# Performance work log

Measured on AMD Instinct MI355X. Metric: run time of the kernel, lower is better.

The kernel has to match this reference:

```python
import jax, jax.numpy as jnp
import numpy as np
import math

EPS = 1e-6
BN_EPS = 1e-5
PI2 = 2.0 * math.pi
NBASIS = 10


def setup_inputs() -> dict:
    key = jax.random.key(0)
    ks = jax.random.split(key, 12)
    nb, nc, ng, ch, npar, out_ch = 4, 512, 2048, 3, 3, 64
    return {
        "x_c": jax.random.normal(ks[0], (nb, nc, ch), jnp.float32),
        "y_c": jax.random.normal(ks[1], (nb, nc, ch), jnp.float32),
        "x_g": jax.random.normal(ks[2], (nb, ng, ch), jnp.float32),
        "sigma": jnp.log(1e-4 + 0.1 * jax.random.uniform(ks[3], (npar,), jnp.float32)),
        "mu": jnp.zeros((npar,), jnp.float32),
        "eps1": jax.random.normal(ks[4], (nb, NBASIS, npar), jnp.float32),
        "b_u": jax.random.uniform(ks[5], (nb, NBASIS, npar), jnp.float32),
        "random_w": jax.random.normal(ks[6], (NBASIS,), jnp.float32),
        "conv_w1": 0.1 * jax.random.normal(ks[7], (ch, 1, 3), jnp.float32),
        "conv_b1": jnp.zeros((ch,), jnp.float32),
        "conv_w2": 0.1 * jax.random.normal(ks[8], (ch, 1, 5), jnp.float32),
        "conv_b2": jnp.zeros((ch,), jnp.float32),
        "conv_w3": 0.1 * jax.random.normal(ks[9], (ch, 1, 9), jnp.float32),
        "conv_b3": jnp.zeros((ch,), jnp.float32),
        "bn_gamma": jnp.ones((npar, ch), jnp.float32),
        "bn_beta": jnp.zeros((npar, ch), jnp.float32),
        "g_w": (1.0 / np.sqrt(2 * npar * ch)) * jax.random.normal(ks[10], (out_ch, 2 * npar * ch), jnp.float32),
        "g_b": jnp.zeros((out_ch,), jnp.float32),
    }


def _dwconv1d(x, w, b, pad):
    # x: (nb, ch, L), w: (ch, 1, ksz) depthwise (groups=ch), cross-correlation like torch
    ch = x.shape[1]
    y = jax.lax.conv_general_dilated(
        x, w, window_strides=(1,), padding=[(pad, pad)],
        dimension_numbers=("NCH", "OIH", "NCH"), feature_group_count=ch)
    return y + b[None, :, None]


def _batchnorm1d(x, gamma, beta):
    # training-mode BN over (batch, length) per channel; x: (nb, ch, L)
    m = x.mean(axis=(0, 2), keepdims=True)
    v = x.var(axis=(0, 2), keepdims=True)  # biased variance (torch normalization)
    return gamma[None, :, None] * (x - m) * jax.lax.rsqrt(v + BN_EPS) + beta[None, :, None]


def reference(x_c, y_c, x_g, sigma, mu, eps1, b_u, random_w,
              conv_w1, conv_b1, conv_w2, conv_b2, conv_w3, conv_b3,
              bn_gamma, bn_beta, g_w, g_b):
    nb, nc, ch = x_c.shape
    ng = x_g.shape[1]
    npar = sigma.shape[0]
    scales = jnp.exp(sigma)  # (npar,)

    # RBF pairwise weights: (nb, nc, ng, ch, npar)
    d = (x_c[:, :, None, :, None] - x_g[:, None, :, :, None]) / (scales + EPS)
    wt = jnp.exp(-0.5 * d * d)
    h0 = wt.sum(axis=1)                                   # (nb, ng, ch, npar)
    h1 = jnp.einsum("bngcp,bnc->bgcp", wt, y_c)           # (nb, ng, ch, npar)
    n_h1 = h1 / (h0 + EPS)

    # random Fourier prior on the grid
    w_mu = jnp.exp(mu)
    w_std = 1.0 / (jnp.exp(sigma) + EPS)
    sample_w = w_mu[None, None, :] + w_std[None, None, :] * eps1  # (nb, nbasis, npar)
    sample_b = PI2 * b_u                                          # (nb, nbasis, npar)
    # Psi: (nb, ng, nbasis, ch, npar)
    psi = jnp.cos(sample_w[:, None, :, None, :] * x_g[:, :, None, :, None]
                  + sample_b[:, None, :, None, :])
    fourier_prior = np.sqrt(2.0 / NBASIS) * jnp.einsum("bgkcp,k->bgcp", psi, random_w)

    n_h1_pos = n_h1 + fourier_prior                        # (nb, ng, ch, npar)

    conv_ws = (conv_w1, conv_w2, conv_w3)
    conv_bs = (conv_b1, conv_b2, conv_b3)
    pads = (1, 2, 4)
    cols = []
    for j in range(npar):
        x = jnp.transpose(n_h1_pos[:, :, :, j], (0, 2, 1))  # (nb, ch, ng)
        x = _dwconv1d(x, conv_ws[j], conv_bs[j], pads[j])
        x = _batchnorm1d(x, bn_gamma[j], bn_beta[j])
        cols.append(jnp.transpose(x, (0, 2, 1)))            # (nb, ng, ch)
    n_h1_pos = jnp.stack(cols, axis=-1)                     # (nb, ng, ch, npar)

    h0_f = h0.reshape(nb, ng, -1)
    n_f = n_h1_pos.reshape(nb, ng, -1)
    feat = jnp.concatenate([h0_f, n_f], axis=-1)            # (nb, ng, 2*ch*npar)
    y_out = feat @ g_w.T + g_b                              # (nb, ng, out_channels)
    return (y_out, n_f, fourier_prior, n_h1, h0_f)
```

## Files before the change

kernel.cpp:

```cpp
#include <hip/hip_runtime.h>
#include <math.h>

#define EPS 1e-6f
#define BN_EPSF 1e-5f
#define PI2F 6.2831853071795864769f
#define LOG2EF 1.4426950408889634f
#define NBB 4
#define NCC 512
#define NGG 2048
#define OUTC 64
#define NBAS 10

#define Y_OFF   0
#define NF_OFF  (NBB*NGG*OUTC)
#define FP_OFF  (NF_OFF  + NBB*NGG*9)
#define NH1_OFF (FP_OFF  + NBB*NGG*9)
#define H0_OFF  (NH1_OFF + NBB*NGG*9)

#define WS_PRE   0
#define WS_CONV  (NBB*9*NGG)
#define WS_STATS (2*NBB*9*NGG)

#if defined(__has_builtin)
# if __has_builtin(__builtin_amdgcn_exp2f)
#  define EXP2F(x) __builtin_amdgcn_exp2f(x)
# endif
#endif
#ifndef EXP2F
# define EXP2F(x) exp2f(x)
#endif

__global__ __launch_bounds__(256) void k1_rbf(
    const float* __restrict__ x_c, const float* __restrict__ y_c,
    const float* __restrict__ x_g, const float* __restrict__ sigma,
    const float* __restrict__ mu, const float* __restrict__ eps1,
    const float* __restrict__ b_u, const float* __restrict__ random_w,
    float* __restrict__ out, float* __restrict__ ws)
{
    const int bid = blockIdx.x;
    const int b = bid >> 8;
    const int gtile = bid & 255;
    const int g0 = gtile * 8;
    const int tid = threadIdx.x;

    __shared__ float cxy[NCC*8 + (NCC/32)*4];
    __shared__ float red[32][8][19];
    __shared__ float sw_l[NBAS*3], sb_l[NBAS*3], rw_l[NBAS];

    const float* xcb = x_c + b*NCC*3;
    const float* ycb = y_c + b*NCC*3;
    for (int i = tid; i < NCC*3; i += 256) {
        int n = i/3, c = i - n*3;
        int base = n*8 + ((n>>5)<<2);
        cxy[base + 2*c]     = xcb[i];
        cxy[base + 2*c + 1] = ycb[i];
    }
    if (tid < NBAS*3) {
        int k = tid/3, p = tid - k*3;
        float wmu  = expf(mu[p]);
        float wstd = 1.0f / (expf(sigma[p]) + EPS);
        sw_l[tid] = wmu + wstd * eps1[(b*NBAS + k)*3 + p];
        sb_l[tid] = PI2F * b_u[(b*NBAS + k)*3 + p];
    }
    if (tid < NBAS) rw_l[tid] = random_w[tid];

    float coef[3];
    #pragma unroll
    for (int p = 0; p < 3; ++p) {
        float s = expf(sigma[p]) + EPS;
        coef[p] = (-0.5f * LOG2EF) / (s*s);
    }

    const int gA = tid & 7;
    const int cA = tid >> 3;
    const float xg0 = x_g[(b*NGG + g0 + gA)*3 + 0];
    const float xg1 = x_g[(b*NGG + g0 + gA)*3 + 1];
    const float xg2 = x_g[(b*NGG + g0 + gA)*3 + 2];

    __syncthreads();

    float h0a[3][3] = {{0}}, h1a[3][3] = {{0}};
    const int fbase = cA*128 + ((cA>>1)<<2);
    #pragma unroll 4
    for (int i = 0; i < 16; ++i) {
        float4 A = *(const float4*)&cxy[fbase + i*8];
        float4 B = *(const float4*)&cxy[fbase + i*8 + 4];
        float d0 = A.x - xg0, d1 = A.z - xg1, d2 = B.x - xg2;
        float dx2[3] = {d0*d0, d1*d1, d2*d2};
        float yv[3]  = {A.y, A.w, B.y};
        #pragma unroll
        for (int c = 0; c < 3; ++c)
            #pragma unroll
            for (int p = 0; p < 3; ++p) {
                float w = EXP2F(dx2[c] * coef[p]);
                h0a[c][p] += w;
                h1a[c][p] += w * yv[c];
            }
    }
    #pragma unroll
    for (int c = 0; c < 3; ++c)
        #pragma unroll
        for (int p = 0; p < 3; ++p) {
            red[cA][gA][c*3 + p]     = h0a[c][p];
            red[cA][gA][9 + c*3 + p] = h1a[c][p];
        }
    __syncthreads();

    if (tid < 72) {
        int gl = tid / 9, cp = tid - gl*9;
        int c = cp / 3, p = cp - c*3;
        float h0 = 0.f, h1 = 0.f;
        #pragma unroll 8
        for (int q = 0; q < 32; ++q) {
            h0 += red[q][gl][cp];
            h1 += red[q][gl][9 + cp];
        }
        float nh1 = h1 / (h0 + EPS);
        float xg = x_g[(b*NGG + g0 + gl)*3 + c];
        float fp = 0.f;
        #pragma unroll
        for (int k = 0; k < NBAS; ++k) {
            float arg = __fadd_rn(__fmul_rn(sw_l[k*3 + p], xg), sb_l[k*3 + p]);
            fp += rw_l[k] * cosf(arg);
        }
        fp *= 0.44721359549995793f;
        int base = (b*NGG + g0 + gl)*9 + cp;
        out[H0_OFF  + base] = h0;
        out[NH1_OFF + base] = nh1;
        out[FP_OFF  + base] = fp;
        ws[WS_PRE + (b*9 + cp)*NGG + g0 + gl] = nh1 + fp;
    }
}

__global__ __launch_bounds__(256) void k2_conv(
    const float* __restrict__ cw1, const float* __restrict__ cb1,
    const float* __restrict__ cw2, const float* __restrict__ cb2,
    const float* __restrict__ cw3, const float* __restrict__ cb3,
    float* __restrict__ ws)
{
    int bid = blockIdx.x;
    int b = bid / 72; int r = bid - b*72;
    int cp = r / 8;  int gc = r - cp*8;
    int g = gc*256 + threadIdx.x;
    int c = cp / 3, p = cp - c*3;
    const float* pre = ws + WS_PRE + (b*9 + cp)*NGG;

    int K, pad; const float* w; float bias;
    if (p == 0)      { K = 3; pad = 1; w = cw1 + c*3; bias = cb1[c]; }
    else if (p == 1) { K = 5; pad = 2; w = cw2 + c*5; bias = cb2[c]; }
    else             { K = 9; pad = 4; w = cw3 + c*9; bias = cb3[c]; }

    float acc = bias;
    for (int k = 0; k < K; ++k) {
        int idx = g - pad + k;
        if (idx >= 0 && idx < NGG) acc += w[k] * pre[idx];
    }
    ws[WS_CONV + (b*9 + cp)*NGG + g] = acc;

    float s1 = acc, s2 = acc*acc;
    #pragma unroll
    for (int o = 32; o > 0; o >>= 1) {
        s1 += __shfl_down(s1, o);
        s2 += __shfl_down(s2, o);
    }
    __shared__ float r1[4], r2[4];
    int lane = threadIdx.x & 63, wv = threadIdx.x >> 6;
    if (lane == 0) { r1[wv] = s1; r2[wv] = s2; }
    __syncthreads();
    if (threadIdx.x == 0) {
        float t1 = r1[0] + r1[1] + r1[2] + r1[3];
        float t2 = r2[0] + r2[1] + r2[2] + r2[3];
        int pidx = cp*32 + b*8 + gc;
        ws[WS_STATS + pidx*2]     = t1;
        ws[WS_STATS + pidx*2 + 1] = t2;
    }
}

__global__ __launch_bounds__(256) void k3_out(
    const float* __restrict__ bn_gamma, const float* __restrict__ bn_beta,
    const float* __restrict__ g_w, const float* __restrict__ g_b,
    float* __restrict__ out, float* __restrict__ ws)
{
    __shared__ float gw_l[OUTC*18];
    __shared__ float feat_l[4][18];
    __shared__ float ps[9][16][2];
    __shared__ float mstat[9][2];
    const int tid = threadIdx.x;

    for (int i = tid; i < OUTC*18; i += 256) gw_l[i] = g_w[i];
    if (tid < 144) {
        int cp = tid / 16, q = tid & 15;
        int idx = WS_STATS + (cp*32 + 2*q)*2;
        ps[cp][q][0] = ws[idx]     + ws[idx + 2];
        ps[cp][q][1] = ws[idx + 1] + ws[idx + 3];
    }
    __syncthreads();
    if (tid < 9) {
        float s1 = 0.f, s2 = 0.f;
        #pragma unroll
        for (int q = 0; q < 16; ++q) { s1 += ps[tid][q][0]; s2 += ps[tid][q][1]; }
        float mean = s1 * (1.0f/8192.0f);
        float var  = s2 * (1.0f/8192.0f) - mean*mean;
        mstat[tid][0] = mean;
        mstat[tid][1] = rsqrtf(var + BN_EPSF);
    }
    __syncthreads();

    if (tid < 72) {
        int pt = tid / 18, j = tid - pt*18;
        int P = blockIdx.x*4 + pt;
        int b = P >> 11, g = P & 2047;
        float f;
        if (j < 9) {
            f = out[H0_OFF + (b*NGG + g)*9 + j];
        } else {
            int cp = j - 9; int c = cp / 3, p = cp - c*3;
            float x = ws[WS_CONV + (b*9 + cp)*NGG + g];
            float v = bn_gamma[p*3 + c] * (x - mstat[cp][0]) * mstat[cp][1]
                      + bn_beta[p*3 + c];
            out[NF_OFF + (b*NGG + g)*9 + cp] = v;
            f = v;
        }
        feat_l[pt][j] = f;
    }
    __syncthreads();

    int pt = tid >> 6, o = tid & 63;
    int P = blockIdx.x*4 + pt;
    int b = P >> 11, g = P & 2047;
    float acc = g_b[o];
    #pragma unroll
    for (int j = 0; j < 18; ++j) acc += feat_l[pt][j] * gw_l[o*18 + j];
    out[Y_OFF + (b*NGG + g)*OUTC + o] = acc;
}

extern "C" void kernel_launch(void* const* d_in, const int* in_sizes, int n_in,
                              void* d_out, int out_size, void* d_ws, size_t ws_size,
                              hipStream_t stream)
{
    const float* x_c      = (const float*)d_in[0];
    const float* y_c      = (const float*)d_in[1];
    const float* x_g      = (const float*)d_in[2];
    const float* sigma    = (const float*)d_in[3];
    const float* mu       = (const float*)d_in[4];
    const float* eps1     = (const float*)d_in[5];
    const float* b_u      = (const float*)d_in[6];
    const float* random_w = (const float*)d_in[7];
    const float* conv_w1  = (const float*)d_in[8];
    const float* conv_b1  = (const float*)d_in[9];
    const float* conv_w2  = (const float*)d_in[10];
    const float* conv_b2  = (const float*)d_in[11];
    const float* conv_w3  = (const float*)d_in[12];
    const float* conv_b3  = (const float*)d_in[13];
    const float* bn_gamma = (const float*)d_in[14];
    const float* bn_beta  = (const float*)d_in[15];
    const float* g_w      = (const float*)d_in[16];
    const float* g_b      = (const float*)d_in[17];

    float* outp = (float*)d_out;
    float* wsp  = (float*)d_ws;

    k1_rbf<<<NBB*256, 256, 0, stream>>>(x_c, y_c, x_g, sigma, mu, eps1, b_u,
                                        random_w, outp, wsp);
    k2_conv<<<NBB*9*(NGG/256), 256, 0, stream>>>(conv_w1, conv_b1, conv_w2, conv_b2,
                                                 conv_w3, conv_b3, wsp);
    k3_out<<<(NBB*NGG)/4, 256, 0, stream>>>(bn_gamma, bn_beta, g_w, g_b, outp, wsp);
}
```

Before: 25.28 us.

## Move Fourier prior and normalization from RBF kernel into conv kernel with shared-memory halo

The RBF kernel now writes only the raw h0/h1 sums to workspace. The Fourier prior, nh1 division and output writes move into the conv kernel, which builds the conv input with halo in shared memory and uses the hardware revolution-based cosine after range reduction. This spreads the cosine work across all threads of the conv blocks instead of 72 threads per RBF block, and lets the conv read neighbours from LDS. The cost is redundant halo recomputation, an extra workspace array, and possible small precision differences from the hardware cosine. The g_w staging in the output kernel also switches to float4 loads.

```diff
diff --git a/kernel.cpp b/kernel.cpp
--- a/kernel.cpp
+++ b/kernel.cpp
@@ -4,6 +4,7 @@
 #define EPS 1e-6f
 #define BN_EPSF 1e-5f
 #define PI2F 6.2831853071795864769f
+#define INV2PIF 0.15915494309189535f
 #define LOG2EF 1.4426950408889634f
 #define NBB 4
 #define NCC 512
@@ -17,25 +18,30 @@
 #define NH1_OFF (FP_OFF  + NBB*NGG*9)
 #define H0_OFF  (NH1_OFF + NBB*NGG*9)
 
-#define WS_PRE   0
-#define WS_CONV  (NBB*9*NGG)
-#define WS_STATS (2*NBB*9*NGG)
+#define WSH0     0
+#define WSH1     (NBB*9*NGG)
+#define WS_CONV  (2*NBB*9*NGG)
+#define WS_STATS (3*NBB*9*NGG)
 
 #if defined(__has_builtin)
 # if __has_builtin(__builtin_amdgcn_exp2f)
 #  define EXP2F(x) __builtin_amdgcn_exp2f(x)
+# endif
+# if __has_builtin(__builtin_amdgcn_cosf)
+#  define COS_REV(r) __builtin_amdgcn_cosf(r)
 # endif
 #endif
 #ifndef EXP2F
 # define EXP2F(x) exp2f(x)
 #endif
+#ifndef COS_REV
+# define COS_REV(r) cosf(PI2F*(r))
+#endif
 
 __global__ __launch_bounds__(256) void k1_rbf(
     const float* __restrict__ x_c, const float* __restrict__ y_c,
     const float* __restrict__ x_g, const float* __restrict__ sigma,
-    const float* __restrict__ mu, const float* __restrict__ eps1,
-    const float* __restrict__ b_u, const float* __restrict__ random_w,
-    float* __restrict__ out, float* __restrict__ ws)
+    float* __restrict__ ws)
 {
     const int bid = blockIdx.x;
     const int b = bid >> 8;
@@ -45,7 +51,6 @@
 
     __shared__ float cxy[NCC*8 + (NCC/32)*4];
     __shared__ float red[32][8][19];
-    __shared__ float sw_l[NBAS*3], sb_l[NBAS*3], rw_l[NBAS];
 
     const float* xcb = x_c + b*NCC*3;
     const float* ycb = y_c + b*NCC*3;
@@ -55,14 +60,6 @@
         cxy[base + 2*c]     = xcb[i];
         cxy[base + 2*c + 1] = ycb[i];
     }
-    if (tid < NBAS*3) {
-        int k = tid/3, p = tid - k*3;
-        float wmu  = expf(mu[p]);
-        float wstd = 1.0f / (expf(sigma[p]) + EPS);
-        sw_l[tid] = wmu + wstd * eps1[(b*NBAS + k)*3 + p];
-        sb_l[tid] = PI2F * b_u[(b*NBAS + k)*3 + p];
-    }
-    if (tid < NBAS) rw_l[tid] = random_w[tid];
 
     float coef[3];
     #pragma unroll
@@ -108,42 +105,75 @@
 
     if (tid < 72) {
         int gl = tid / 9, cp = tid - gl*9;
-        int c = cp / 3, p = cp - c*3;
         float h0 = 0.f, h1 = 0.f;
         #pragma unroll 8
         for (int q = 0; q < 32; ++q) {
             h0 += red[q][gl][cp];
             h1 += red[q][gl][9 + cp];
         }
-        float nh1 = h1 / (h0 + EPS);
-        float xg = x_g[(b*NGG + g0 + gl)*3 + c];
-        float fp = 0.f;
-        #pragma unroll
-        for (int k = 0; k < NBAS; ++k) {
-            float arg = __fadd_rn(__fmul_rn(sw_l[k*3 + p], xg), sb_l[k*3 + p]);
-            fp += rw_l[k] * cosf(arg);
-        }
-        fp *= 0.44721359549995793f;
-        int base = (b*NGG + g0 + gl)*9 + cp;
-        out[H0_OFF  + base] = h0;
-        out[NH1_OFF + base] = nh1;
-        out[FP_OFF  + base] = fp;
-        ws[WS_PRE + (b*9 + cp)*NGG + g0 + gl] = nh1 + fp;
-    }
-}
-
-__global__ __launch_bounds__(256) void k2_conv(
+        int idx = (b*9 + cp)*NGG + g0 + gl;
+        ws[WSH0 + idx] = h0;
+        ws[WSH1 + idx] = h1;
+    }
+}
+
+__global__ __launch_bounds__(256) void k2_fin_conv(
+    const float* __restrict__ x_g, const float* __restrict__ sigma,
+    const float* __restrict__ mu, const float* __restrict__ eps1,
+    const float* __restrict__ b_u, const float* __restrict__ random_w,
     const float* __restrict__ cw1, const float* __restrict__ cb1,
     const float* __restrict__ cw2, const float* __restrict__ cb2,
     const float* __restrict__ cw3, const float* __restrict__ cb3,
-    float* __restrict__ ws)
-{
-    int bid = blockIdx.x;
-    int b = bid / 72; int r = bid - b*72;
-    int cp = r / 8;  int gc = r - cp*8;
-    int g = gc*256 + threadIdx.x;
-    int c = cp / 3, p = cp - c*3;
-    const float* pre = ws + WS_PRE + (b*9 + cp)*NGG;
+    float* __restrict__ out, float* __restrict__ ws)
+{
+    const int bid = blockIdx.x;
+    const int b = bid / 72; int r = bid - b*72;
+    const int cp = r >> 3;  const int gc = r & 7;
+    const int c = cp / 3, p = cp - c*3;
+    const int tid = threadIdx.x;
+
+    __shared__ float pre_l[264];
+    __shared__ float swl[NBAS], sbl[NBAS], rwl[NBAS];
+    __shared__ float r1[4], r2[4];
+
+    if (tid < NBAS) {
+        float wmu  = expf(mu[p]);
+        float wstd = 1.0f / (expf(sigma[p]) + EPS);
+        swl[tid] = wmu + wstd * eps1[(b*NBAS + tid)*3 + p];
+        sbl[tid] = PI2F * b_u[(b*NBAS + tid)*3 + p];
+        rwl[tid] = random_w[tid];
+    }
+    __syncthreads();
+
+    for (int s = tid; s < 264; s += 256) {
+        int gf = gc*256 - 4 + s;
+        float v = 0.f;
+        if (gf >= 0 && gf < NGG) {
+            int idx = (b*9 + cp)*NGG + gf;
+            float h0 = ws[WSH0 + idx];
+            float h1 = ws[WSH1 + idx];
+            float nh1 = h1 / (h0 + EPS);
+            float xg = x_g[(b*NGG + gf)*3 + c];
+            float fp = 0.f;
+            #pragma unroll
+            for (int k = 0; k < NBAS; ++k) {
+                float arg = __fadd_rn(__fmul_rn(swl[k], xg), sbl[k]);
+                float rev = arg * INV2PIF;
+                rev = rev - floorf(rev);
+                fp += rwl[k] * COS_REV(rev);
+            }
+            fp *= 0.44721359549995793f;
+            v = nh1 + fp;
+            if (s >= 4 && s < 260) {
+                int obase = (b*NGG + gf)*9 + cp;
+                out[H0_OFF  + obase] = h0;
+                out[NH1_OFF + obase] = nh1;
+                out[FP_OFF  + obase] = fp;
+            }
+        }
+        pre_l[s] = v;
+    }
+    __syncthreads();
 
     int K, pad; const float* w; float bias;
     if (p == 0)      { K = 3; pad = 1; w = cw1 + c*3; bias = cb1[c]; }
@@ -151,11 +181,9 @@
     else             { K = 9; pad = 4; w = cw3 + c*9; bias = cb3[c]; }
 
     float acc = bias;
-    for (int k = 0; k < K; ++k) {
-        int idx = g - pad + k;
-        if (idx >= 0 && idx < NGG) acc += w[k] * pre[idx];
-    }
-    ws[WS_CONV + (b*9 + cp)*NGG + g] = acc;
+    for (int k = 0; k < K; ++k)
+        acc += w[k] * pre_l[tid + 4 - pad + k];
+    ws[WS_CONV + (b*9 + cp)*NGG + gc*256 + tid] = acc;
 
     float s1 = acc, s2 = acc*acc;
     #pragma unroll
@@ -163,11 +191,10 @@
         s1 += __shfl_down(s1, o);
         s2 += __shfl_down(s2, o);
     }
-    __shared__ float r1[4], r2[4];
-    int lane = threadIdx.x & 63, wv = threadIdx.x >> 6;
+    int lane = tid & 63, wv = tid >> 6;
     if (lane == 0) { r1[wv] = s1; r2[wv] = s2; }
     __syncthreads();
-    if (threadIdx.x == 0) {
+    if (tid == 0) {
         float t1 = r1[0] + r1[1] + r1[2] + r1[3];
         float t2 = r2[0] + r2[1] + r2[2] + r2[3];
         int pidx = cp*32 + b*8 + gc;
@@ -181,13 +208,15 @@
     const float* __restrict__ g_w, const float* __restrict__ g_b,
     float* __restrict__ out, float* __restrict__ ws)
 {
-    __shared__ float gw_l[OUTC*18];
+    __shared__ float4 gw4[OUTC*18/4];
     __shared__ float feat_l[4][18];
     __shared__ float ps[9][16][2];
     __shared__ float mstat[9][2];
     const int tid = threadIdx.x;
-
-    for (int i = tid; i < OUTC*18; i += 256) gw_l[i] = g_w[i];
+    float* gw_l = (float*)gw4;
+
+    for (int i = tid; i < OUTC*18/4; i += 256)
+        gw4[i] = ((const float4*)g_w)[i];
     if (tid < 144) {
         int cp = tid / 16, q = tid & 15;
         int idx = WS_STATS + (cp*32 + 2*q)*2;
@@ -260,9 +289,10 @@
     float* outp = (float*)d_out;
     float* wsp  = (float*)d_ws;
 
-    k1_rbf<<<NBB*256, 256, 0, stream>>>(x_c, y_c, x_g, sigma, mu, eps1, b_u,
-                                        random_w, outp, wsp);
-    k2_conv<<<NBB*9*(NGG/256), 256, 0, stream>>>(conv_w1, conv_b1, conv_w2, conv_b2,
-                                                 conv_w3, conv_b3, wsp);
+    k1_rbf<<<NBB*256, 256, 0, stream>>>(x_c, y_c, x_g, sigma, wsp);
+    k2_fin_conv<<<NBB*9*(NGG/256), 256, 0, stream>>>(x_g, sigma, mu, eps1, b_u,
+                                                     random_w, conv_w1, conv_b1,
+                                                     conv_w2, conv_b2, conv_w3,
+                                                     conv_b3, outp, wsp);
     k3_out<<<(NBB*NGG)/4, 256, 0, stream>>>(bn_gamma, bn_beta, g_w, g_b, outp, wsp);
 }
```

New measurement: 23.77 us. 1.06x faster.
